# Kernel tuning notes

Hardware: AMD Instinct MI355X
Metric: run time of the kernel (lower is better)

The kernel has to match this reference:

```python
import jax, jax.numpy as jnp
import numpy as np

B, S, HID = 2, 2048, 2048
H, KV, HD, RD = 16, 4, 128, 64
MAX_POS = 4096
FULL = HD + RD  # 192


def precompute_rope(dim, max_len, theta=10000.0):
    freqs = 1.0 / (theta ** (jnp.arange(0, dim, 2, dtype=jnp.float32) / dim))
    t = jnp.arange(max_len, dtype=jnp.float32)
    f = jnp.outer(t, freqs)  # (max_len, dim//2)
    return jnp.cos(f), jnp.sin(f)


def apply_rope(x, cos, sin):
    # Faithful to the torch source: uses x.shape[-2] (which is the HEAD axis
    # for (B,S,H,rd) layout) to slice the rope cache, and broadcasts over it.
    n = x.shape[-2]
    c = cos[:n]
    s = sin[:n]
    x1 = x[..., ::2]
    x2 = x[..., 1::2]
    out1 = x1 * c - x2 * s
    out2 = x1 * s + x2 * c
    return jnp.stack([out1, out2], axis=-1).reshape(x.shape)


def setup_inputs() -> dict:
    key = jax.random.key(0)
    ks = jax.random.split(key, 8)
    sc = 0.02
    return {
        "hidden_states": jax.random.normal(ks[0], (B, S, HID), jnp.float32),
        "Wq": jax.random.normal(ks[1], (HID, H * HD), jnp.float32) * sc,
        "Wkvc": jax.random.normal(ks[2], (HID, 512), jnp.float32) * sc,
        "Wkdec": jax.random.normal(ks[3], (512, KV * HD), jnp.float32) * sc,
        "Wvdec": jax.random.normal(ks[4], (512, KV * HD), jnp.float32) * sc,
        "Wqrope": jax.random.normal(ks[5], (HID, H * RD), jnp.float32) * sc,
        "Wkrope": jax.random.normal(ks[6], (512, KV * RD), jnp.float32) * sc,
        "Wo": jax.random.normal(ks[7], (H * FULL, HID), jnp.float32) * sc,
    }


def reference(hidden_states, Wq, Wkvc, Wkdec, Wvdec, Wqrope, Wkrope, Wo):
    b, s, _ = hidden_states.shape
    ratio = H // KV
    cos, sin = precompute_rope(RD, MAX_POS)

    q_nope = (hidden_states @ Wq).reshape(b, s, H, HD)
    q_rope = apply_rope((hidden_states @ Wqrope).reshape(b, s, H, RD), cos, sin)

    c = hidden_states @ Wkvc  # (b, s, d_c) low-rank latent
    k_nope = (c @ Wkdec).reshape(b, s, KV, HD)
    v = (c @ Wvdec).reshape(b, s, KV, HD)
    k_rope = apply_rope((c @ Wkrope).reshape(b, s, KV, RD), cos, sin)

    q = jnp.concatenate([q_nope, q_rope], axis=-1)  # (b,s,H,FULL)
    k = jnp.concatenate([k_nope, k_rope], axis=-1)  # (b,s,KV,FULL)
    v_p = jnp.pad(v, ((0, 0), (0, 0), (0, 0), (0, RD)))  # (b,s,KV,FULL)

    # GQA expand: each kv head repeated `ratio` times contiguously
    k = jnp.repeat(k, ratio, axis=2)      # (b,s,H,FULL)
    v_p = jnp.repeat(v_p, ratio, axis=2)  # (b,s,H,FULL)

    scale = 1.0 / jnp.sqrt(jnp.asarray(FULL, dtype=q.dtype))
    scores = jnp.einsum("bqhd,bkhd->bhqk", q, k) * scale
    causal = jnp.tril(jnp.ones((s, s), dtype=bool))
    scores = jnp.where(causal[None, None], scores, jnp.finfo(scores.dtype).min)
    attn = jax.nn.softmax(scores, axis=-1)
    out = jnp.einsum("bhqk,bkhd->bqhd", attn, v_p).reshape(b, s, H * FULL)
    return out @ Wo
```

## Files before the change

### kernel.cpp

```cpp
#include <hip/hip_runtime.h>
#include <hip/hip_bf16.h>
#include <stdint.h>


typedef __bf16 bf16;
typedef __bf16 bf16x8 __attribute__((ext_vector_type(8)));
typedef __bf16 bf16x4 __attribute__((ext_vector_type(4)));
typedef float f32x4 __attribute__((ext_vector_type(4)));

#define GAS __attribute__((address_space(1)))
#define LAS __attribute__((address_space(3)))

__device__ __forceinline__ void gload16(const void* g, void* l) {
  __builtin_amdgcn_global_load_lds((GAS void*)(g), (LAS void*)(l), 16, 0, 0);
}

__device__ __forceinline__ f32x4 mfma16(bf16x8 a, bf16x8 b, f32x4 c) {
  return __builtin_amdgcn_mfma_f32_16x16x32_bf16(a, b, c, 0, 0, 0);
}

template<int CTRL>
__device__ __forceinline__ float dppmov(float x) {
  int v = __builtin_amdgcn_update_dpp(0, __float_as_int(x), CTRL, 0xF, 0xF, false);
  return __int_as_float(v);
}
__device__ __forceinline__ float rowmax16(float x) {
  x = fmaxf(x, dppmov<0x128>(x));
  x = fmaxf(x, dppmov<0x124>(x));
  x = fmaxf(x, dppmov<0x122>(x));
  x = fmaxf(x, dppmov<0x121>(x));
  return x;
}
__device__ __forceinline__ float rowsum16(float x) {
  x += dppmov<0x128>(x);
  x += dppmov<0x124>(x);
  x += dppmov<0x122>(x);
  x += dppmov<0x121>(x);
  return x;
}

template<bool V> struct BoolC { static constexpr bool v = V; };

#define OFF_XB    0ull
#define OFF_WQT   (OFF_XB    + 16777216ull)
#define OFF_WQRT  (OFF_WQT   + 8388608ull)
#define OFF_WKVCT (OFF_WQRT  + 4194304ull)
#define OFF_WKDT  (OFF_WKVCT + 2097152ull)
#define OFF_WVDT  (OFF_WKDT  + 524288ull)
#define OFF_WKRT  (OFF_WVDT  + 524288ull)
#define OFF_WOT   (OFF_WKRT  + 262144ull)
#define OFF_CB    (OFF_WOT   + 8388608ull)
#define OFF_QBUF  (OFF_CB    + 4194304ull)
#define OFF_KBUF  (OFF_QBUF  + 25165824ull)
#define OFF_VT    (OFF_KBUF  + 6291456ull)
#define OFF_QRR   (OFF_VT    + 4194304ull)
#define OFF_KRR   (OFF_QRR   + 8388608ull)
#define OFF_OBUF  (OFF_KRR   + 2097152ull)

#define QSCALE 0.07216878364870323f

__global__ void cast_x_kernel(const float* __restrict__ in, bf16* __restrict__ out, int n4) {
  int i = blockIdx.x * blockDim.x + threadIdx.x;
  int stride = gridDim.x * blockDim.x;
  for (; i < n4; i += stride) {
    float4 v = reinterpret_cast<const float4*>(in)[i];
    bf16x4 o;
    o[0] = (bf16)v.x; o[1] = (bf16)v.y; o[2] = (bf16)v.z; o[3] = (bf16)v.w;
    reinterpret_cast<bf16x4*>(out)[i] = o;
  }
}

struct TDescs {
  const float* in[7];
  bf16* out[7];
  int Kd[7], Nd[7], gather[7];
  int tile0[8];
};

__global__ void transpose_cast_fused(TDescs D) {
  __shared__ float t[32][33];
  int bid = blockIdx.x;
  int m = 0;
  while (bid >= D.tile0[m + 1]) m++;
  int local = bid - D.tile0[m];
  const float* in = D.in[m];
  bf16* out = D.out[m];
  int Kd = D.Kd[m], Nd = D.Nd[m], gather = D.gather[m];
  int txn = Nd >> 5;
  int n0 = (local % txn) * 32, k0 = (local / txn) * 32;
  int tx = threadIdx.x, ty = threadIdx.y;
#pragma unroll
  for (int i = 0; i < 4; i++) {
    int k = k0 + ty + i * 8;
    int kr = gather ? ((k >> 7) * 192 + (k & 127)) : k;
    t[ty + i * 8][tx] = in[(size_t)kr * Nd + n0 + tx];
  }
  __syncthreads();
#pragma unroll
  for (int i = 0; i < 4; i++) {
    int n = n0 + ty + i * 8;
    out[(size_t)n * Kd + k0 + tx] = (bf16)t[tx][ty + i * 8];
  }
}

template<int MODE>
__global__ __launch_bounds__(256, 2)
void gemm_bt(const bf16* __restrict__ A, const bf16* __restrict__ BT,
             void* __restrict__ out0, void* __restrict__ out1, void* __restrict__ out2,
             int M, int N, int K) {
  __shared__ bf16 ldsA[128 * 32];
  __shared__ bf16 ldsB[128 * 32];
  const int tid = threadIdx.x;
  const int wid = tid >> 6, lane = tid & 63;
  const int lr = lane & 15, lg = lane >> 4;
  const int wr = wid >> 1, wc = wid & 1;
  const int m0 = blockIdx.y * 128, n0 = blockIdx.x * 128;

  const int rowA = tid >> 2;
  const int cg = (tid & 3) ^ (rowA & 3);
  const int slot = lg ^ (lane & 3);

  const f32x4 fzero = {0.f, 0.f, 0.f, 0.f};
  f32x4 acc[4][4];
#pragma unroll
  for (int m = 0; m < 4; m++)
#pragma unroll
    for (int n = 0; n < 4; n++) acc[m][n] = fzero;

  const int nk = K >> 5;
  for (int kt = 0; kt < nk; kt++) {
    const int kb = kt * 32 + cg * 8;
#pragma unroll
    for (int r = 0; r < 2; r++) {
      gload16(&A[(size_t)(m0 + r * 64 + rowA) * K + kb], &ldsA[r * 2048 + wid * 512]);
      gload16(&BT[(size_t)(n0 + r * 64 + rowA) * K + kb], &ldsB[r * 2048 + wid * 512]);
    }
    __syncthreads();
    bf16x8 af[4], bfr[4];
#pragma unroll
    for (int m = 0; m < 4; m++)
      af[m] = *reinterpret_cast<const bf16x8*>(&ldsA[(wr * 64 + m * 16 + lr) * 32 + slot * 8]);
#pragma unroll
    for (int n = 0; n < 4; n++)
      bfr[n] = *reinterpret_cast<const bf16x8*>(&ldsB[(wc * 64 + n * 16 + lr) * 32 + slot * 8]);
#pragma unroll
    for (int m = 0; m < 4; m++)
#pragma unroll
      for (int n = 0; n < 4; n++) acc[m][n] = mfma16(af[m], bfr[n], acc[m][n]);
    __syncthreads();
  }

#pragma unroll
  for (int m = 0; m < 4; m++)
#pragma unroll
    for (int n = 0; n < 4; n++)
#pragma unroll
      for (int i = 0; i < 4; i++) {
        int row = m0 + wr * 64 + m * 16 + 4 * lg + i;
        int col = n0 + wc * 64 + n * 16 + lr;
        float v = acc[m][n][i];
        int b = row >> 11, s = row & 2047;
        if (MODE == 1) {
          ((float*)out0)[(size_t)row * N + col] = v;
        } else if (MODE == 6) {
          if (col < 2048) {
            int h = col >> 7, d = col & 127;
            ((bf16*)out0)[((size_t)(b * 16 + h) * 2048 + s) * 192 + d] = (bf16)(v * QSCALE);
          } else if (col < 3072) {
            ((bf16*)out1)[(size_t)row * 1024 + (col - 2048)] = (bf16)v;
          } else {
            ((bf16*)out2)[(size_t)row * 512 + (col - 3072)] = (bf16)v;
          }
        } else if (MODE == 7) {
          if (col < 512) {
            int kv = col >> 7, d = col & 127;
            ((bf16*)out0)[((size_t)(b * 4 + kv) * 2048 + s) * 192 + d] = (bf16)v;
          } else if (col < 1024) {
            int mm = col - 512, kv = mm >> 7, d = mm & 127;
            ((bf16*)out1)[((size_t)(b * 4 + kv) * 128 + d) * 2048 + s] = (bf16)v;
          } else {
            ((bf16*)out2)[(size_t)row * 256 + (col - 1024)] = (bf16)v;
          }
        }
      }
}

__global__ void rope_q_kernel(const bf16* __restrict__ raw, bf16* __restrict__ qbuf) {
  int idx = blockIdx.x * 256 + threadIdx.x;
  int i = idx & 31;
  int h = (idx >> 5) & 15;
  int rs = idx >> 9;
  int b = rs >> 11, s = rs & 2047;
  float x1 = (float)raw[(size_t)rs * 1024 + h * 64 + 2 * i];
  float x2 = (float)raw[(size_t)rs * 1024 + h * 64 + 2 * i + 1];
  float freq = __expf(-(float)(2 * i) * (9.210340371976184f / 64.f));
  float ang = (float)h * freq;
  float sn, cs;
  __sincosf(ang, &sn, &cs);
  size_t o = ((size_t)(b * 16 + h) * 2048 + s) * 192 + 128 + 2 * i;
  qbuf[o] = (bf16)((x1 * cs - x2 * sn) * QSCALE);
  qbuf[o + 1] = (bf16)((x1 * sn + x2 * cs) * QSCALE);
}

__global__ void rope_k_kernel(const bf16* __restrict__ raw, bf16* __restrict__ kbuf) {
  int idx = blockIdx.x * 256 + threadIdx.x;
  int i = idx & 31;
  int kv = (idx >> 5) & 3;
  int rs = idx >> 7;
  int b = rs >> 11, s = rs & 2047;
  float x1 = (float)raw[(size_t)rs * 256 + kv * 64 + 2 * i];
  float x2 = (float)raw[(size_t)rs * 256 + kv * 64 + 2 * i + 1];
  float freq = __expf(-(float)(2 * i) * (9.210340371976184f / 64.f));
  float ang = (float)kv * freq;
  float sn, cs;
  __sincosf(ang, &sn, &cs);
  size_t o = ((size_t)(b * 4 + kv) * 2048 + s) * 192 + 128 + 2 * i;
  kbuf[o] = (bf16)(x1 * cs - x2 * sn);
  kbuf[o + 1] = (bf16)(x1 * sn + x2 * cs);
}

__global__ __launch_bounds__(256, 2)
void attn_kernel(const bf16* __restrict__ qbuf, const bf16* __restrict__ kbuf,
                 const bf16* __restrict__ vt, bf16* __restrict__ obuf) {
  __shared__ __align__(16) char Klds[24576];
  __shared__ __align__(16) char Vlds[16384];
  __shared__ __align__(16) bf16 PldsA[4][16][72];
  __shared__ __align__(16) bf16 PldsB[4][16][72];

  const int tid = threadIdx.x;
  const int wid = tid >> 6, lane = tid & 63;
  const int lr = lane & 15, lg = lane >> 4;
  const int px = blockIdx.x, h = blockIdx.y, b = blockIdx.z;
  const int bxB = 31 - px;
  const int qrbA = px * 64 + wid * 16, qrbB = bxB * 64 + wid * 16;
  const bf16* Q = qbuf + (size_t)(b * 16 + h) * 2048 * 192;
  const char* Kg = (const char*)(kbuf + (size_t)(b * 4 + (h >> 2)) * 2048 * 192);
  const char* Vg = (const char*)(vt + (size_t)(b * 4 + (h >> 2)) * 128 * 2048);

  int koff[6], voff[4];
#pragma unroll
  for (int c = 0; c < 6; c++) {
    int o = (wid * 6 + c) * 1024 + lane * 16;
    koff[c] = o ^ ((lane >> 3) << 4);
  }
#pragma unroll
  for (int c = 0; c < 4; c++) {
    int o = (wid * 4 + c) * 1024 + lane * 16;
    int d = o >> 7;
    voff[c] = d * 4096 + (((lane & 7) * 16) ^ ((lane >> 3) << 4));
  }
  const int xk0 = ((3 * lr + 0) & 7) << 4;
  const int xk1 = ((3 * lr + 1) & 7) << 4;
  const int xk2 = ((3 * lr + 2) & 7) << 4;
  const int xv  = (lr & 7) << 4;

  bf16x8 qfA[6], qfB[6];
#pragma unroll
  for (int kk = 0; kk < 6; kk++) {
    qfA[kk] = *reinterpret_cast<const bf16x8*>(&Q[(size_t)(qrbA + lr) * 192 + kk * 32 + lg * 8]);
    qfB[kk] = *reinterpret_cast<const bf16x8*>(&Q[(size_t)(qrbB + lr) * 192 + kk * 32 + lg * 8]);
  }

  const f32x4 fzero = {0.f, 0.f, 0.f, 0.f};
  f32x4 accA[8], accB[8];
#pragma unroll
  for (int nn = 0; nn < 8; nn++) { accA[nn] = fzero; accB[nn] = fzero; }
  float mA[4] = {-1e30f, -1e30f, -1e30f, -1e30f};
  float mB[4] = {-1e30f, -1e30f, -1e30f, -1e30f};
  float lA[4] = {0.f, 0.f, 0.f, 0.f};
  float lB[4] = {0.f, 0.f, 0.f, 0.f};

  auto softmax = [&](f32x4* sacc, float* mrow, float* lsum, f32x4* acco,
                     bf16 (*P)[72], int diag, int qrb, int k0) {
    float fsv[4];
    int grow = 0;
#pragma unroll
    for (int i = 0; i < 4; i++) {
      const int row = qrb + 4 * lg + i;
      float s[4];
#pragma unroll
      for (int n = 0; n < 4; n++) s[n] = sacc[n][i];
      if (diag) {
#pragma unroll
        for (int n = 0; n < 4; n++)
          if (k0 + n * 16 + lr > row) s[n] = -1e30f;
      }
      float mx = rowmax16(fmaxf(fmaxf(s[0], s[1]), fmaxf(s[2], s[3])));
      int g = mx > mrow[i] + 8.f;
      float mnew = g ? mx : mrow[i];
      float fs = g ? __expf(mrow[i] - mx) : 1.f;
      grow |= g;
      fsv[i] = fs;
      float p[4], sum = 0.f;
#pragma unroll
      for (int n = 0; n < 4; n++) { p[n] = __expf(s[n] - mnew); sum += p[n]; }
      sum = rowsum16(sum);
      mrow[i] = mnew;
      lsum[i] = lsum[i] * fs + sum;
#pragma unroll
      for (int n = 0; n < 4; n++) P[4 * lg + i][n * 16 + lr] = (bf16)p[n];
    }
    if (__any(grow)) {
#pragma unroll
      for (int nn = 0; nn < 8; nn++)
#pragma unroll
        for (int i = 0; i < 4; i++) acco[nn][i] *= fsv[i];
    }
  };

  auto tile_body = [&](auto DC, int j, int diagA, int diagB) {
    constexpr bool DUAL = decltype(DC)::v;
    const char* Kt = Kg + (size_t)j * 24576;
    const char* Vtb = Vg + (size_t)j * 128;
#pragma unroll
    for (int c = 0; c < 6; c++)
      gload16(Kt + koff[c], Klds + (wid * 6 + c) * 1024);
#pragma unroll
    for (int c = 0; c < 4; c++)
      gload16(Vtb + voff[c], Vlds + (wid * 4 + c) * 1024);
    __syncthreads();

    const int k0 = j * 64;
    f32x4 sA[4], sB[4];
#pragma unroll
    for (int n = 0; n < 4; n++) { sA[n] = fzero; sB[n] = fzero; }
    __builtin_amdgcn_s_setprio(1);
#pragma unroll
    for (int n = 0; n < 4; n++) {
      const int rb = (n * 16 + lr) * 384;
#pragma unroll
      for (int kk = 0; kk < 6; kk++) {
        const int x = (kk < 2) ? xk0 : ((kk < 4) ? xk1 : xk2);
        bf16x8 kf = *reinterpret_cast<const bf16x8*>(Klds + rb + ((kk * 64 + lg * 16) ^ x));
        sB[n] = mfma16(qfB[kk], kf, sB[n]);
        if constexpr (DUAL) sA[n] = mfma16(qfA[kk], kf, sA[n]);
      }
    }
    __builtin_amdgcn_s_setprio(0);

    softmax(sB, mB, lB, accB, PldsB[wid], diagB, qrbB, k0);
    if constexpr (DUAL) softmax(sA, mA, lA, accA, PldsA[wid], diagA, qrbA, k0);

    __builtin_amdgcn_s_setprio(1);
#pragma unroll
    for (int ks = 0; ks < 2; ks++) {
      bf16x8 pfB = *reinterpret_cast<const bf16x8*>(&PldsB[wid][lr][ks * 32 + lg * 8]);
      bf16x8 pfA;
      if constexpr (DUAL)
        pfA = *reinterpret_cast<const bf16x8*>(&PldsA[wid][lr][ks * 32 + lg * 8]);
#pragma unroll
      for (int nn = 0; nn < 8; nn++) {
        bf16x8 vf = *reinterpret_cast<const bf16x8*>(
            Vlds + (nn * 16 + lr) * 128 + ((ks * 64 + lg * 16) ^ xv));
        accB[nn] = mfma16(pfB, vf, accB[nn]);
        if constexpr (DUAL) accA[nn] = mfma16(pfA, vf, accA[nn]);
      }
    }
    __builtin_amdgcn_s_setprio(0);
    __syncthreads();
  };

  for (int j = 0; j <= px; j++) tile_body(BoolC<true>{}, j, j == px, 0);
  for (int j = px + 1; j <= bxB; j++) tile_body(BoolC<false>{}, j, 0, j == bxB);

#pragma unroll
  for (int i = 0; i < 4; i++) { lA[i] = 1.f / lA[i]; lB[i] = 1.f / lB[i]; }
#pragma unroll
  for (int nn = 0; nn < 8; nn++)
#pragma unroll
    for (int i = 0; i < 4; i++) {
      int rowA = qrbA + 4 * lg + i, rowB = qrbB + 4 * lg + i;
      obuf[(size_t)(b * 2048 + rowA) * 2048 + h * 128 + nn * 16 + lr] = (bf16)(accA[nn][i] * lA[i]);
      obuf[(size_t)(b * 2048 + rowB) * 2048 + h * 128 + nn * 16 + lr] = (bf16)(accB[nn][i] * lB[i]);
    }
}

extern "C" void kernel_launch(void* const* d_in, const int* in_sizes, int n_in,
                              void* d_out, int out_size, void* d_ws, size_t ws_size,
                              hipStream_t stream) {
  (void)in_sizes; (void)n_in; (void)out_size; (void)ws_size;
  const float* Xf     = (const float*)d_in[0];
  const float* Wq     = (const float*)d_in[1];
  const float* Wkvc   = (const float*)d_in[2];
  const float* Wkdec  = (const float*)d_in[3];
  const float* Wvdec  = (const float*)d_in[4];
  const float* Wqrope = (const float*)d_in[5];
  const float* Wkrope = (const float*)d_in[6];
  const float* Wo     = (const float*)d_in[7];
  float* Out = (float*)d_out;
  char* ws = (char*)d_ws;

  bf16* Xb     = (bf16*)(ws + OFF_XB);
  bf16* WqT    = (bf16*)(ws + OFF_WQT);
  bf16* WqrT   = (bf16*)(ws + OFF_WQRT);
  bf16* WkvcT  = (bf16*)(ws + OFF_WKVCT);
  bf16* WkdT   = (bf16*)(ws + OFF_WKDT);
  bf16* WvdT   = (bf16*)(ws + OFF_WVDT);
  bf16* WkrT   = (bf16*)(ws + OFF_WKRT);
  bf16* WoT    = (bf16*)(ws + OFF_WOT);
  bf16* Cb     = (bf16*)(ws + OFF_CB);
  bf16* Qbuf   = (bf16*)(ws + OFF_QBUF);
  bf16* Kbuf   = (bf16*)(ws + OFF_KBUF);
  bf16* Vt     = (bf16*)(ws + OFF_VT);
  bf16* Qrr    = (bf16*)(ws + OFF_QRR);
  bf16* Krr    = (bf16*)(ws + OFF_KRR);
  bf16* Obuf   = (bf16*)(ws + OFF_OBUF);

  cast_x_kernel<<<2048, 256, 0, stream>>>(Xf, Xb, (4096 * 2048) / 4);

  TDescs D;
  const float* ins[7] = {Wq, Wqrope, Wkvc, Wkdec, Wvdec, Wkrope, Wo};
  bf16* outs[7] = {WqT, WqrT, WkvcT, WkdT, WvdT, WkrT, WoT};
  int kds[7] = {2048, 2048, 2048, 512, 512, 512, 2048};
  int nds[7] = {2048, 1024, 512, 512, 512, 256, 2048};
  int gts[7] = {0, 0, 0, 0, 0, 0, 1};
  int acc_t = 0;
  for (int m = 0; m < 7; m++) {
    D.in[m] = ins[m]; D.out[m] = outs[m];
    D.Kd[m] = kds[m]; D.Nd[m] = nds[m]; D.gather[m] = gts[m];
    D.tile0[m] = acc_t;
    acc_t += (nds[m] / 32) * (kds[m] / 32);
  }
  D.tile0[7] = acc_t;
  transpose_cast_fused<<<acc_t, dim3(32, 8), 0, stream>>>(D);

  gemm_bt<6><<<dim3(28, 32), 256, 0, stream>>>(Xb, WqT, Qbuf, Qrr, Cb, 4096, 3584, 2048);
  gemm_bt<7><<<dim3(10, 32), 256, 0, stream>>>(Cb, WkdT, Kbuf, Vt, Krr, 4096, 1280, 512);

  rope_q_kernel<<<8192, 256, 0, stream>>>(Qrr, Qbuf);
  rope_k_kernel<<<2048, 256, 0, stream>>>(Krr, Kbuf);

  attn_kernel<<<dim3(16, 16, 2), 256, 0, stream>>>(Qbuf, Kbuf, Vt, Obuf);

  gemm_bt<1><<<dim3(16, 32), 256, 0, stream>>>(Obuf, WoT, Out, nullptr, nullptr, 4096, 2048, 2048);
}
```

Baseline: 377.9 us.

## Fuse RoPE into GEMM epilogues, merge x cast into prep, slim attention LDS

RoPE for q and k is now applied in the GEMM epilogues, using a DPP lane-pair swap to fetch the partner element, and the rotated values are written straight into Qbuf/Kbuf. This removes the two standalone rope kernels and their intermediate buffers. The x fp32-to-bf16 cast is folded into the fused weight-prep kernel as a plain-copy mode, saving one launch. In attention, the Q scale now includes log2(e) so softmax can use exp2, and P shares one LDS buffer with PV run per side. Launch bounds are raised to 3 blocks per CU to lift occupancy, at the risk of register spills.

Result: slower. 410.1 us (+8.5%).

```diff
diff --git a/kernel.cpp b/kernel.cpp
--- a/kernel.cpp
+++ b/kernel.cpp
@@ -37,6 +37,9 @@
   x += dppmov<0x122>(x);
   x += dppmov<0x121>(x);
   return x;
+}
+__device__ __forceinline__ float pairswap(float x) {
+  return dppmov<0xB1>(x);
 }
 
 template<bool V> struct BoolC { static constexpr bool v = V; };
@@ -53,31 +56,18 @@
 #define OFF_QBUF  (OFF_CB    + 4194304ull)
 #define OFF_KBUF  (OFF_QBUF  + 25165824ull)
 #define OFF_VT    (OFF_KBUF  + 6291456ull)
-#define OFF_QRR   (OFF_VT    + 4194304ull)
-#define OFF_KRR   (OFF_QRR   + 8388608ull)
-#define OFF_OBUF  (OFF_KRR   + 2097152ull)
-
-#define QSCALE 0.07216878364870323f
-
-__global__ void cast_x_kernel(const float* __restrict__ in, bf16* __restrict__ out, int n4) {
-  int i = blockIdx.x * blockDim.x + threadIdx.x;
-  int stride = gridDim.x * blockDim.x;
-  for (; i < n4; i += stride) {
-    float4 v = reinterpret_cast<const float4*>(in)[i];
-    bf16x4 o;
-    o[0] = (bf16)v.x; o[1] = (bf16)v.y; o[2] = (bf16)v.z; o[3] = (bf16)v.w;
-    reinterpret_cast<bf16x4*>(out)[i] = o;
-  }
-}
+#define OFF_OBUF  (OFF_VT    + 4194304ull)
+
+#define QSCALE2 0.10412902090772143f
 
 struct TDescs {
-  const float* in[7];
-  bf16* out[7];
-  int Kd[7], Nd[7], gather[7];
-  int tile0[8];
+  const float* in[8];
+  bf16* out[8];
+  int Kd[8], Nd[8], gather[8];
+  int tile0[9];
 };
 
-__global__ void transpose_cast_fused(TDescs D) {
+__global__ void prep_fused(TDescs D) {
   __shared__ float t[32][33];
   int bid = blockIdx.x;
   int m = 0;
@@ -89,10 +79,18 @@
   int txn = Nd >> 5;
   int n0 = (local % txn) * 32, k0 = (local / txn) * 32;
   int tx = threadIdx.x, ty = threadIdx.y;
+  if (gather == 2) {
+#pragma unroll
+    for (int i = 0; i < 4; i++) {
+      size_t idx = (size_t)(k0 + ty + i * 8) * Nd + n0 + tx;
+      out[idx] = (bf16)in[idx];
+    }
+    return;
+  }
 #pragma unroll
   for (int i = 0; i < 4; i++) {
     int k = k0 + ty + i * 8;
-    int kr = gather ? ((k >> 7) * 192 + (k & 127)) : k;
+    int kr = (gather == 1) ? ((k >> 7) * 192 + (k & 127)) : k;
     t[ty + i * 8][tx] = in[(size_t)kr * Nd + n0 + tx];
   }
   __syncthreads();
@@ -165,9 +163,18 @@
         } else if (MODE == 6) {
           if (col < 2048) {
             int h = col >> 7, d = col & 127;
-            ((bf16*)out0)[((size_t)(b * 16 + h) * 2048 + s) * 192 + d] = (bf16)(v * QSCALE);
+            ((bf16*)out0)[((size_t)(b * 16 + h) * 2048 + s) * 192 + d] = (bf16)(v * QSCALE2);
           } else if (col < 3072) {
-            ((bf16*)out1)[(size_t)row * 1024 + (col - 2048)] = (bf16)v;
+            int col2 = col - 2048;
+            int hh = col2 >> 6, r = col2 & 63, ii = r >> 1;
+            float part = pairswap(v);
+            float freq = __expf(-(float)(2 * ii) * (9.210340371976184f / 64.f));
+            float sn, cs;
+            __sincosf((float)hh * freq, &sn, &cs);
+            float x1 = (lr & 1) ? part : v;
+            float x2 = (lr & 1) ? v : part;
+            float o = (lr & 1) ? (x1 * sn + x2 * cs) : (x1 * cs - x2 * sn);
+            ((bf16*)out0)[((size_t)(b * 16 + hh) * 2048 + s) * 192 + 128 + r] = (bf16)(o * QSCALE2);
           } else {
             ((bf16*)out2)[(size_t)row * 512 + (col - 3072)] = (bf16)v;
           }
@@ -179,53 +186,27 @@
             int mm = col - 512, kv = mm >> 7, d = mm & 127;
             ((bf16*)out1)[((size_t)(b * 4 + kv) * 128 + d) * 2048 + s] = (bf16)v;
           } else {
-            ((bf16*)out2)[(size_t)row * 256 + (col - 1024)] = (bf16)v;
+            int col2 = col - 1024;
+            int kv = col2 >> 6, r = col2 & 63, ii = r >> 1;
+            float part = pairswap(v);
+            float freq = __expf(-(float)(2 * ii) * (9.210340371976184f / 64.f));
+            float sn, cs;
+            __sincosf((float)kv * freq, &sn, &cs);
+            float x1 = (lr & 1) ? part : v;
+            float x2 = (lr & 1) ? v : part;
+            float o = (lr & 1) ? (x1 * sn + x2 * cs) : (x1 * cs - x2 * sn);
+            ((bf16*)out0)[((size_t)(b * 4 + kv) * 2048 + s) * 192 + 128 + r] = (bf16)o;
           }
         }
       }
 }
 
-__global__ void rope_q_kernel(const bf16* __restrict__ raw, bf16* __restrict__ qbuf) {
-  int idx = blockIdx.x * 256 + threadIdx.x;
-  int i = idx & 31;
-  int h = (idx >> 5) & 15;
-  int rs = idx >> 9;
-  int b = rs >> 11, s = rs & 2047;
-  float x1 = (float)raw[(size_t)rs * 1024 + h * 64 + 2 * i];
-  float x2 = (float)raw[(size_t)rs * 1024 + h * 64 + 2 * i + 1];
-  float freq = __expf(-(float)(2 * i) * (9.210340371976184f / 64.f));
-  float ang = (float)h * freq;
-  float sn, cs;
-  __sincosf(ang, &sn, &cs);
-  size_t o = ((size_t)(b * 16 + h) * 2048 + s) * 192 + 128 + 2 * i;
-  qbuf[o] = (bf16)((x1 * cs - x2 * sn) * QSCALE);
-  qbuf[o + 1] = (bf16)((x1 * sn + x2 * cs) * QSCALE);
-}
-
-__global__ void rope_k_kernel(const bf16* __restrict__ raw, bf16* __restrict__ kbuf) {
-  int idx = blockIdx.x * 256 + threadIdx.x;
-  int i = idx & 31;
-  int kv = (idx >> 5) & 3;
-  int rs = idx >> 7;
-  int b = rs >> 11, s = rs & 2047;
-  float x1 = (float)raw[(size_t)rs * 256 + kv * 64 + 2 * i];
-  float x2 = (float)raw[(size_t)rs * 256 + kv * 64 + 2 * i + 1];
-  float freq = __expf(-(float)(2 * i) * (9.210340371976184f / 64.f));
-  float ang = (float)kv * freq;
-  float sn, cs;
-  __sincosf(ang, &sn, &cs);
-  size_t o = ((size_t)(b * 4 + kv) * 2048 + s) * 192 + 128 + 2 * i;
-  kbuf[o] = (bf16)(x1 * cs - x2 * sn);
-  kbuf[o + 1] = (bf16)(x1 * sn + x2 * cs);
-}
-
-__global__ __launch_bounds__(256, 2)
+__global__ __launch_bounds__(256, 3)
 void attn_kernel(const bf16* __restrict__ qbuf, const bf16* __restrict__ kbuf,
                  const bf16* __restrict__ vt, bf16* __restrict__ obuf) {
   __shared__ __align__(16) char Klds[24576];
   __shared__ __align__(16) char Vlds[16384];
-  __shared__ __align__(16) bf16 PldsA[4][16][72];
-  __shared__ __align__(16) bf16 PldsB[4][16][72];
+  __shared__ __align__(16) bf16 Plds[4][16][72];
 
   const int tid = threadIdx.x;
   const int wid = tid >> 6, lane = tid & 63;
@@ -271,7 +252,7 @@
   float lB[4] = {0.f, 0.f, 0.f, 0.f};
 
   auto softmax = [&](f32x4* sacc, float* mrow, float* lsum, f32x4* acco,
-                     bf16 (*P)[72], int diag, int qrb, int k0) {
+                     int diag, int qrb, int k0) {
     float fsv[4];
     int grow = 0;
 #pragma unroll
@@ -288,17 +269,17 @@
       float mx = rowmax16(fmaxf(fmaxf(s[0], s[1]), fmaxf(s[2], s[3])));
       int g = mx > mrow[i] + 8.f;
       float mnew = g ? mx : mrow[i];
-      float fs = g ? __expf(mrow[i] - mx) : 1.f;
+      float fs = g ? __builtin_exp2f(mrow[i] - mx) : 1.f;
       grow |= g;
       fsv[i] = fs;
       float p[4], sum = 0.f;
 #pragma unroll
-      for (int n = 0; n < 4; n++) { p[n] = __expf(s[n] - mnew); sum += p[n]; }
+      for (int n = 0; n < 4; n++) { p[n] = __builtin_exp2f(s[n] - mnew); sum += p[n]; }
       sum = rowsum16(sum);
       mrow[i] = mnew;
       lsum[i] = lsum[i] * fs + sum;
 #pragma unroll
-      for (int n = 0; n < 4; n++) P[4 * lg + i][n * 16 + lr] = (bf16)p[n];
+      for (int n = 0; n < 4; n++) Plds[wid][4 * lg + i][n * 16 + lr] = (bf16)p[n];
     }
     if (__any(grow)) {
 #pragma unroll
@@ -306,6 +287,21 @@
 #pragma unroll
         for (int i = 0; i < 4; i++) acco[nn][i] *= fsv[i];
     }
+  };
+
+  auto pv = [&](f32x4* acco) {
+    __builtin_amdgcn_s_setprio(1);
+#pragma unroll
+    for (int ks = 0; ks < 2; ks++) {
+      bf16x8 pf = *reinterpret_cast<const bf16x8*>(&Plds[wid][lr][ks * 32 + lg * 8]);
+#pragma unroll
+      for (int nn = 0; nn < 8; nn++) {
+        bf16x8 vf = *reinterpret_cast<const bf16x8*>(
+            Vlds + (nn * 16 + lr) * 128 + ((ks * 64 + lg * 16) ^ xv));
+        acco[nn] = mfma16(pf, vf, acco[nn]);
+      }
+    }
+    __builtin_amdgcn_s_setprio(0);
   };
 
   auto tile_body = [&](auto DC, int j, int diagA, int diagB) {
@@ -338,25 +334,12 @@
     }
     __builtin_amdgcn_s_setprio(0);
 
-    softmax(sB, mB, lB, accB, PldsB[wid], diagB, qrbB, k0);
-    if constexpr (DUAL) softmax(sA, mA, lA, accA, PldsA[wid], diagA, qrbA, k0);
-
-    __builtin_amdgcn_s_setprio(1);
-#pragma unroll
-    for (int ks = 0; ks < 2; ks++) {
-      bf16x8 pfB = *reinterpret_cast<const bf16x8*>(&PldsB[wid][lr][ks * 32 + lg * 8]);
-      bf16x8 pfA;
-      if constexpr (DUAL)
-        pfA = *reinterpret_cast<const bf16x8*>(&PldsA[wid][lr][ks * 32 + lg * 8]);
-#pragma unroll
-      for (int nn = 0; nn < 8; nn++) {
-        bf16x8 vf = *reinterpret_cast<const bf16x8*>(
-            Vlds + (nn * 16 + lr) * 128 + ((ks * 64 + lg * 16) ^ xv));
-        accB[nn] = mfma16(pfB, vf, accB[nn]);
-        if constexpr (DUAL) accA[nn] = mfma16(pfA, vf, accA[nn]);
-      }
-    }
-    __builtin_amdgcn_s_setprio(0);
+    softmax(sB, mB, lB, accB, diagB, qrbB, k0);
+    pv(accB);
+    if constexpr (DUAL) {
+      softmax(sA, mA, lA, accA, diagA, qrbA, k0);
+      pv(accA);
+    }
     __syncthreads();
   };
 
@@ -402,33 +385,26 @@
   bf16* Qbuf   = (bf16*)(ws + OFF_QBUF);
   bf16* Kbuf   = (bf16*)(ws + OFF_KBUF);
   bf16* Vt     = (bf16*)(ws + OFF_VT);
-  bf16* Qrr    = (bf16*)(ws + OFF_QRR);
-  bf16* Krr    = (bf16*)(ws + OFF_KRR);
   bf16* Obuf   = (bf16*)(ws + OFF_OBUF);
 
-  cast_x_kernel<<<2048, 256, 0, stream>>>(Xf, Xb, (4096 * 2048) / 4);
-
   TDescs D;
-  const float* ins[7] = {Wq, Wqrope, Wkvc, Wkdec, Wvdec, Wkrope, Wo};
-  bf16* outs[7] = {WqT, WqrT, WkvcT, WkdT, WvdT, WkrT, WoT};
-  int kds[7] = {2048, 2048, 2048, 512, 512, 512, 2048};
-  int nds[7] = {2048, 1024, 512, 512, 512, 256, 2048};
-  int gts[7] = {0, 0, 0, 0, 0, 0, 1};
+  const float* ins[8] = {Wq, Wqrope, Wkvc, Wkdec, Wvdec, Wkrope, Wo, Xf};
+  bf16* outs[8] = {WqT, WqrT, WkvcT, WkdT, WvdT, WkrT, WoT, Xb};
+  int kds[8] = {2048, 2048, 2048, 512, 512, 512, 2048, 4096};
+  int nds[8] = {2048, 1024, 512, 512, 512, 256, 2048, 2048};
+  int gts[8] = {0, 0, 0, 0, 0, 0, 1, 2};
   int acc_t = 0;
-  for (int m = 0; m < 7; m++) {
+  for (int m = 0; m < 8; m++) {
     D.in[m] = ins[m]; D.out[m] = outs[m];
     D.Kd[m] = kds[m]; D.Nd[m] = nds[m]; D.gather[m] = gts[m];
     D.tile0[m] = acc_t;
     acc_t += (nds[m] / 32) * (kds[m] / 32);
   }
-  D.tile0[7] = acc_t;
-  transpose_cast_fused<<<acc_t, dim3(32, 8), 0, stream>>>(D);
-
-  gemm_bt<6><<<dim3(28, 32), 256, 0, stream>>>(Xb, WqT, Qbuf, Qrr, Cb, 4096, 3584, 2048);
-  gemm_bt<7><<<dim3(10, 32), 256, 0, stream>>>(Cb, WkdT, Kbuf, Vt, Krr, 4096, 1280, 512);
-
-  rope_q_kernel<<<8192, 256, 0, stream>>>(Qrr, Qbuf);
-  rope_k_kernel<<<2048, 256, 0, stream>>>(Krr, Kbuf);
+  D.tile0[8] = acc_t;
+  prep_fused<<<acc_t, dim3(32, 8), 0, stream>>>(D);
+
+  gemm_bt<6><<<dim3(28, 32), 256, 0, stream>>>(Xb, WqT, Qbuf, nullptr, Cb, 4096, 3584, 2048);
+  gemm_bt<7><<<dim3(10, 32), 256, 0, stream>>>(Cb, WkdT, Kbuf, Vt, nullptr, 4096, 1280, 512);
 
   attn_kernel<<<dim3(16, 16, 2), 256, 0, stream>>>(Qbuf, Kbuf, Vt, Obuf);
 
```
